# Kernel optimization log

Hardware: AMD Instinct MI355X
Metric: run time of the kernel (lower is better)

Reference implementation:

```python
import jax, jax.numpy as jnp
import numpy as np

B, H, W, C = 8, 64, 64, 256
CB = C // 2          # bottleneck_dim = channels // 2
COMPRESSION = 2      # max-pool factor on flattened spatial axis of phi and g


def setup_inputs() -> dict:
    key = jax.random.key(0)
    k = jax.random.split(key, 5)
    he = lambda kk, fan_in, shape: jax.random.normal(kk, shape, jnp.float32) * np.sqrt(2.0 / fan_in)
    return {
        "x": jax.random.normal(k[0], (B, H, W, C), jnp.float32),
        "W_theta": he(k[1], C, (C, CB)),
        "W_phi": he(k[2], C, (C, CB)),
        "W_g": he(k[3], C, (C, CB)),
        "W_out": he(k[4], CB, (CB, C)),
    }


def _maxpool1d(t, pool):
    # MaxPool1D(pool) along axis 1 of [B, N, C] (valid padding, stride=pool)
    b, n, c = t.shape
    return t.reshape(b, n // pool, pool, c).max(axis=2)


def reference(x, W_theta, W_phi, W_g, W_out):
    b, h, w, c = x.shape
    n = h * w
    xf = x.reshape(b, n, c)                      # flatten spatial dims
    theta = xf @ W_theta                         # [B, N, Cb] (1x1 conv, no bias)
    phi = _maxpool1d(xf @ W_phi, COMPRESSION)    # [B, N/2, Cb]
    g = _maxpool1d(xf @ W_g, COMPRESSION)        # [B, N/2, Cb]
    f = jax.nn.softmax(jnp.einsum('bnd,bmd->bnm', theta, phi), axis=-1)  # [B, N, N/2]
    y = jnp.einsum('bnm,bmd->bnd', f, g)         # [B, N, Cb]
    y = (y @ W_out).reshape(b, h, w, c)          # expand conv back to C
    return x + y                                 # add_residual=True
```

## Files before the change

kernel.cpp:

```cpp
#include <hip/hip_runtime.h>
#include <math.h>

#define BB 8
#define NN 4096
#define MM 2048
#define CC 256
#define CBD 128

typedef __attribute__((ext_vector_type(8))) short s16x8;
typedef __attribute__((ext_vector_type(4))) float f32x4;
typedef __attribute__((ext_vector_type(16))) float f32x16;
typedef unsigned short u16;
typedef unsigned int u32;

__device__ __forceinline__ u16 f2bf(float f) {
    union { float f; u32 u; } v; v.f = f;
    u32 r = v.u + 0x7fffu + ((v.u >> 16) & 1u);
    return (u16)(r >> 16);
}
__device__ __forceinline__ float bf2f(u16 h) {
    union { u32 u; float f; } v; v.u = ((u32)h) << 16; return v.f;
}
__device__ __forceinline__ u32 asu(float f) {
    union { float f; u32 u; } v; v.f = f; return v.u;
}
__device__ __forceinline__ u32 pkbf(float lo, float hi) {
    return __builtin_amdgcn_perm(asu(hi), asu(lo), 0x07060302u);
}

#define MFMA(a, b, c)   __builtin_amdgcn_mfma_f32_16x16x32_bf16(a, b, c, 0, 0, 0)
#define MFMA32(a, b, c) __builtin_amdgcn_mfma_f32_32x32x16_bf16(a, b, c, 0, 0, 0)

__device__ __forceinline__ void gload_lds16(const u16* g, u16* l) {
    __builtin_amdgcn_global_load_lds(
        (const __attribute__((address_space(1))) void*)g,
        (__attribute__((address_space(3))) void*)l, 16, 0, 0);
}

__global__ __launch_bounds__(256) void k_split_w(
    const float* __restrict__ wt, const float* __restrict__ wp,
    const float* __restrict__ wg, const float* __restrict__ wo,
    u16* wth, u16* wtl, u16* wph, u16* wpl, u16* wgh, u16* wgl, u16* wot) {
    int e = blockIdx.x * 256 + threadIdx.x;
    int m = blockIdx.y;
    if (m < 3) {
        const float* src = m == 0 ? wt : (m == 1 ? wp : wg);
        u16* oh = m == 0 ? wth : (m == 1 ? wph : wgh);
        u16* ol = m == 0 ? wtl : (m == 1 ? wpl : wgl);
        int r = e >> 7, c = e & 127;
        float f = src[e];
        u16 hi = f2bf(f);
        oh[c * 256 + r] = hi;
        ol[c * 256 + r] = f2bf(f - bf2f(hi));
    } else {
        int r = e >> 8, c = e & 255;
        wot[c * 128 + r] = f2bf(wo[e]);
    }
}

__global__ __launch_bounds__(256) void k_proj(
    const float* __restrict__ x,
    const u16* __restrict__ wth, const u16* __restrict__ wtl,
    const u16* __restrict__ wph, const u16* __restrict__ wpl,
    const u16* __restrict__ wgh,
    u16* __restrict__ th, u16* __restrict__ tl,
    u16* __restrict__ ph, u16* __restrict__ pl, u16* __restrict__ gt) {
    __shared__ u16 sxh[64][40], sxl[64][40];
    __shared__ u16 sw[5][128][40];
    int tid = threadIdx.x;
    int w = tid >> 6, lane = tid & 63, q = lane >> 4, li = lane & 15;
    int r0 = blockIdx.x * 64;
    int wr2 = (w >> 1) * 32, wcc = (w & 1) * 64;
    const u16* Ws[5] = {wth, wtl, wph, wpl, wgh};

    f32x4 aT[2][4], aP[2][4], aG[2][4];
#pragma unroll
    for (int i = 0; i < 2; i++)
#pragma unroll
        for (int j = 0; j < 4; j++) {
            aT[i][j] = (f32x4)0.f; aP[i][j] = (f32x4)0.f; aG[i][j] = (f32x4)0.f;
        }

    for (int kc = 0; kc < 8; kc++) {
        {
            int row = tid >> 2, seg = tid & 3;
            const float* xp = &x[(size_t)(r0 + row) * 256 + kc * 32 + seg * 8];
            float4 v0 = ((const float4*)xp)[0];
            float4 v1 = ((const float4*)xp)[1];
            float vv[8] = {v0.x, v0.y, v0.z, v0.w, v1.x, v1.y, v1.z, v1.w};
            u16 hh[8], ll[8];
#pragma unroll
            for (int t = 0; t < 8; t++) {
                hh[t] = f2bf(vv[t]);
                ll[t] = f2bf(vv[t] - bf2f(hh[t]));
            }
            *(s16x8*)&sxh[row][seg * 8] = *(s16x8*)&hh[0];
            *(s16x8*)&sxl[row][seg * 8] = *(s16x8*)&ll[0];
        }
#pragma unroll
        for (int u = 0; u < 10; u++) {
            int mat = u >> 1;
            int col = (u & 1) * 64 + (tid >> 2), ch = tid & 3;
            s16x8 v = *(const s16x8*)&Ws[mat][(size_t)col * 256 + kc * 32 + ch * 8];
            *(s16x8*)&sw[mat][col][ch * 8] = v;
        }
        __syncthreads();

        s16x8 ah[2], al[2];
#pragma unroll
        for (int i = 0; i < 2; i++) {
            ah[i] = *(const s16x8*)&sxh[wr2 + i * 16 + li][q * 8];
            al[i] = *(const s16x8*)&sxl[wr2 + i * 16 + li][q * 8];
        }
#pragma unroll
        for (int j = 0; j < 4; j++) {
            int col = wcc + j * 16 + li;
            s16x8 bth = *(const s16x8*)&sw[0][col][q * 8];
            s16x8 btl = *(const s16x8*)&sw[1][col][q * 8];
            s16x8 bph = *(const s16x8*)&sw[2][col][q * 8];
            s16x8 bpl = *(const s16x8*)&sw[3][col][q * 8];
            s16x8 bgh = *(const s16x8*)&sw[4][col][q * 8];
#pragma unroll
            for (int i = 0; i < 2; i++) {
                aT[i][j] = MFMA(ah[i], bth, aT[i][j]);
                aT[i][j] = MFMA(al[i], bth, aT[i][j]);
                aT[i][j] = MFMA(ah[i], btl, aT[i][j]);
                aP[i][j] = MFMA(ah[i], bph, aP[i][j]);
                aP[i][j] = MFMA(al[i], bph, aP[i][j]);
                aP[i][j] = MFMA(ah[i], bpl, aP[i][j]);
                aG[i][j] = MFMA(ah[i], bgh, aG[i][j]);
                aG[i][j] = MFMA(al[i], bgh, aG[i][j]);
            }
        }
        __syncthreads();
    }

#pragma unroll
    for (int i = 0; i < 2; i++)
#pragma unroll
        for (int j = 0; j < 4; j++) {
            int col = wcc + j * 16 + li;
#pragma unroll
            for (int reg = 0; reg < 4; reg++) {
                int n = r0 + wr2 + i * 16 + q * 4 + reg;
                float v = aT[i][j][reg];
                u16 hi = f2bf(v);
                th[(size_t)n * 128 + col] = hi;
                tl[(size_t)n * 128 + col] = f2bf(v - bf2f(hi));
            }
#pragma unroll
            for (int pr = 0; pr < 2; pr++) {
                int n = r0 + wr2 + i * 16 + q * 4 + pr * 2;
                int mrow = n >> 1;
                float vp = fmaxf(aP[i][j][pr * 2], aP[i][j][pr * 2 + 1]);
                u16 hi = f2bf(vp);
                ph[(size_t)mrow * 128 + col] = hi;
                pl[(size_t)mrow * 128 + col] = f2bf(vp - bf2f(hi));
                float vg = fmaxf(aG[i][j][pr * 2], aG[i][j][pr * 2 + 1]);
                int b = n >> 12;
                int mi = mrow & 2047;
                int mi2 = (mi & ~12) | ((mi & 4) << 1) | ((mi & 8) >> 1);
                gt[(size_t)b * (128 * 2048) + (size_t)col * 2048 + mi2] = f2bf(vg);
            }
        }
}

__global__ __launch_bounds__(256, 2) void k_attn(
    const u16* __restrict__ th, const u16* __restrict__ tl,
    const u16* __restrict__ ph, const u16* __restrict__ pl,
    const u16* __restrict__ gt, u16* __restrict__ ot,
    float* __restrict__ Mv, float* __restrict__ Lv) {
    __shared__ u16 smem[24576];
    u16* skh = smem;
    u16* skl = smem + 8192;
    u16* sg  = smem + 16384;
    int tid = threadIdx.x, w = tid >> 6, lane = tid & 63;
    int q = lane & 31, b = lane >> 5;
    int bb = blockIdx.y;
    int s = blockIdx.x & 1;
    int qt = blockIdx.x >> 1;
    int n0 = qt * 128;
    int row128 = w * 32 + q;
    size_t qrow = ((size_t)bb * 4096 + n0 + row128) * 128;

    s16x8 Qh[8], Ql[8];
#pragma unroll
    for (int ks = 0; ks < 8; ks++) {
        Qh[ks] = *(const s16x8*)&th[qrow + ks * 16 + b * 8];
        Ql[ks] = *(const s16x8*)&tl[qrow + ks * 16 + b * 8];
    }
    float mrow = -INFINITY, lrow = 0.f;
    f32x16 o[4];
#pragma unroll
    for (int c = 0; c < 4; c++) o[c] = (f32x16)0.f;

    int r_hi = lane >> 4, c_hi = lane & 15;
    int r_lo = lane >> 3, c_lo = lane & 7;
    int k0 = s * 1024;

    for (int kt = 0; kt < 16; kt++) {
        int m0 = k0 + kt * 64;
        if (kt) __syncthreads();
#pragma unroll
        for (int jj = 0; jj < 4; jj++) {
            int r = w * 16 + jj * 4 + r_hi;
            int gc = c_hi ^ (r & 7);
            size_t ga = (((size_t)(bb * 2048 + m0 + r)) << 7) + gc * 8;
            gload_lds16(&ph[ga], &skh[(w * 16 + jj * 4) << 7]);
            gload_lds16(&pl[ga], &skl[(w * 16 + jj * 4) << 7]);
            int r2 = w * 32 + jj * 8 + r_lo;
            int gc2 = c_lo ^ (r2 & 7);
            size_t ga2 = (size_t)bb * (128 * 2048) + (size_t)r2 * 2048 + m0 + gc2 * 8;
            gload_lds16(&gt[ga2], &sg[(w * 32 + jj * 8) << 6]);
        }
        __syncthreads();

        f32x16 S[2];
        S[0] = (f32x16)0.f; S[1] = (f32x16)0.f;
#pragma unroll
        for (int ks = 0; ks < 8; ks++) {
            int off0 = (q << 7) + (((ks * 2 + b) ^ (q & 7)) << 3);
            int r1 = 32 + q;
            int off1 = (r1 << 7) + (((ks * 2 + b) ^ (r1 & 7)) << 3);
            s16x8 ah0 = *(const s16x8*)&skh[off0];
            s16x8 al0 = *(const s16x8*)&skl[off0];
            s16x8 ah1 = *(const s16x8*)&skh[off1];
            s16x8 al1 = *(const s16x8*)&skl[off1];
            S[0] = MFMA32(ah0, Qh[ks], S[0]);
            S[1] = MFMA32(ah1, Qh[ks], S[1]);
            S[0] = MFMA32(al0, Qh[ks], S[0]);
            S[1] = MFMA32(al1, Qh[ks], S[1]);
            S[0] = MFMA32(ah0, Ql[ks], S[0]);
            S[1] = MFMA32(ah1, Ql[ks], S[1]);
        }

        float vmax = S[0][0];
#pragma unroll
        for (int r = 0; r < 16; r++) {
            vmax = fmaxf(vmax, S[0][r]);
            vmax = fmaxf(vmax, S[1][r]);
        }
        vmax = fmaxf(vmax, __shfl_xor(vmax, 32, 64));
        float nm = fmaxf(mrow, vmax);
        float alph = __expf(mrow - nm);
        mrow = nm;
        float rs = 0.f;
#pragma unroll
        for (int r = 0; r < 16; r++) {
            float p0 = __expf(S[0][r] - nm); S[0][r] = p0; rs += p0;
            float p1 = __expf(S[1][r] - nm); S[1][r] = p1; rs += p1;
        }
        rs += __shfl_xor(rs, 32, 64);
        lrow = lrow * alph + rs;
#pragma unroll
        for (int c = 0; c < 4; c++)
#pragma unroll
            for (int r = 0; r < 16; r++) o[c][r] *= alph;

#pragma unroll
        for (int t = 0; t < 4; t++) {
            int half = t >> 1, base = (t & 1) * 8;
            s16x8 Pf;
            u32* pf = (u32*)&Pf;
#pragma unroll
            for (int r2 = 0; r2 < 4; r2++)
                pf[r2] = pkbf(S[half][base + 2 * r2], S[half][base + 2 * r2 + 1]);
#pragma unroll
            for (int c = 0; c < 4; c++) {
                int ch = c * 32 + q;
                int off = (ch << 6) + (((t * 2 + b) ^ (ch & 7)) << 3);
                s16x8 gv = *(const s16x8*)&sg[off];
                o[c] = MFMA32(gv, Pf, o[c]);
            }
        }
    }
    __syncthreads();

    u16* sc = smem;
#pragma unroll
    for (int c = 0; c < 4; c++)
#pragma unroll
        for (int r2 = 0; r2 < 8; r2++) {
            int ch = c * 32 + ((r2 & 1) << 1) + 8 * (r2 >> 1) + 4 * b;
            u32 pk = (u32)f2bf(o[c][2 * r2]) | ((u32)f2bf(o[c][2 * r2 + 1]) << 16);
            *(u32*)&sc[row128 * 136 + ch] = pk;
        }
    __syncthreads();
    size_t obase = ((size_t)s * 32768 + (size_t)bb * 4096 + n0) * 128;
    int rowy = tid >> 1;
#pragma unroll
    for (int j = 0; j < 8; j++) {
        int chk = (tid & 1) * 8 + j;
        s16x8 v = *(const s16x8*)&sc[rowy * 136 + chk * 8];
        *(s16x8*)&ot[obase + (size_t)rowy * 128 + chk * 8] = v;
    }
    if (b == 0) {
        int gi = s * 32768 + bb * 4096 + n0 + row128;
        Mv[gi] = mrow;
        Lv[gi] = lrow;
    }
}

__global__ __launch_bounds__(256) void k_out(
    const u16* __restrict__ ot, const float* __restrict__ Mv,
    const float* __restrict__ Lv, const u16* __restrict__ wot,
    const float* __restrict__ x, float* __restrict__ out) {
    __shared__ char lds_o[36864];
    u16 (*sy)[72] = (u16(*)[72])lds_o;
    u16 (*sw)[72] = (u16(*)[72])(lds_o + 18432);
    int tid = threadIdx.x, w = tid >> 6, lane = tid & 63, q = lane >> 4, li = lane & 15;
    int r0 = blockIdx.x * 128, c0 = blockIdx.y * 128;
    int wr = (w >> 1) * 64, wc = (w & 1) * 64;
    const size_t OS = (size_t)32768 * 128;

    float a1v[4], a2v[4];
#pragma unroll
    for (int i = 0; i < 4; i++) {
        int gr = r0 + ((tid + i * 256) >> 3);
        float m1 = Mv[gr], m2 = Mv[32768 + gr];
        float l1 = Lv[gr], l2 = Lv[32768 + gr];
        float Mx = fmaxf(m1, m2);
        float e1 = __expf(m1 - Mx), e2 = __expf(m2 - Mx);
        float inv = 1.f / (l1 * e1 + l2 * e2);
        a1v[i] = e1 * inv;
        a2v[i] = e2 * inv;
    }

    f32x4 acc[4][4];
#pragma unroll
    for (int i = 0; i < 4; i++)
#pragma unroll
        for (int j = 0; j < 4; j++) acc[i][j] = (f32x4)0.f;

    for (int kc = 0; kc < 2; kc++) {
#pragma unroll
        for (int i = 0; i < 4; i++) {
            int ch = tid + i * 256;
            int r = ch >> 3, cc = (ch & 7) * 8;
            size_t ga = (size_t)(r0 + r) * 128 + kc * 64 + cc;
            s16x8 o1 = *(const s16x8*)&ot[ga];
            s16x8 o2 = *(const s16x8*)&ot[OS + ga];
            s16x8 yv;
#pragma unroll
            for (int e = 0; e < 8; e++)
                yv[e] = (short)f2bf(bf2f((u16)o1[e]) * a1v[i] +
                                    bf2f((u16)o2[e]) * a2v[i]);
            *(s16x8*)&sy[r][cc] = yv;
            *(s16x8*)&sw[r][cc] = *(const s16x8*)&wot[(size_t)(c0 + r) * 128 + kc * 64 + cc];
        }
        __syncthreads();
#pragma unroll
        for (int ks = 0; ks < 2; ks++)
#pragma unroll
            for (int i = 0; i < 4; i++) {
                s16x8 a = *(const s16x8*)&sy[wr + i * 16 + li][ks * 32 + q * 8];
#pragma unroll
                for (int j = 0; j < 4; j++) {
                    s16x8 bv = *(const s16x8*)&sw[wc + j * 16 + li][ks * 32 + q * 8];
                    acc[i][j] = MFMA(a, bv, acc[i][j]);
                }
            }
        __syncthreads();
    }

    float* sT = (float*)lds_o;
#pragma unroll
    for (int h = 0; h < 2; h++) {
        __syncthreads();
        if ((w >> 1) == h) {
#pragma unroll
            for (int i = 0; i < 4; i++)
#pragma unroll
                for (int j = 0; j < 4; j++)
#pragma unroll
                    for (int reg = 0; reg < 4; reg++)
                        sT[(i * 16 + q * 4 + reg) * 132 + wc + j * 16 + li] =
                            acc[i][j][reg];
        }
        __syncthreads();
#pragma unroll
        for (int p = 0; p < 8; p++) {
            int r = (tid >> 5) + p * 8;
            int c4 = (tid & 31) * 4;
            f32x4 yv = *(f32x4*)&sT[r * 132 + c4];
            size_t row = (size_t)(r0 + h * 64 + r);
            float4 xv = *(const float4*)&x[row * 256 + c0 + c4];
            float4 ov;
            ov.x = xv.x + yv[0]; ov.y = xv.y + yv[1];
            ov.z = xv.z + yv[2]; ov.w = xv.w + yv[3];
            *(float4*)&out[row * 256 + c0 + c4] = ov;
        }
    }
}

extern "C" void kernel_launch(void* const* d_in, const int* in_sizes, int n_in,
                              void* d_out, int out_size, void* d_ws, size_t ws_size,
                              hipStream_t stream) {
    const float* x  = (const float*)d_in[0];
    const float* wt = (const float*)d_in[1];
    const float* wp = (const float*)d_in[2];
    const float* wg = (const float*)d_in[3];
    const float* wo = (const float*)d_in[4];
    float* out = (float*)d_out;

    char* p = (char*)d_ws;
    auto alloc = [&](size_t bytes) {
        char* r = p;
        p += (bytes + 255) & ~(size_t)255;
        return r;
    };
    const size_t NT = (size_t)BB * NN * CBD;
    const size_t NP = (size_t)BB * MM * CBD;

    u16* wth = (u16*)alloc(CC * CBD * 2);
    u16* wtl = (u16*)alloc(CC * CBD * 2);
    u16* wph = (u16*)alloc(CC * CBD * 2);
    u16* wpl = (u16*)alloc(CC * CBD * 2);
    u16* wgh = (u16*)alloc(CC * CBD * 2);
    u16* wgl = (u16*)alloc(CC * CBD * 2);
    u16* wot = (u16*)alloc(CC * CBD * 2);
    u16* th  = (u16*)alloc(NT * 2);
    u16* tl  = (u16*)alloc(NT * 2);
    u16* ph  = (u16*)alloc(NP * 2);
    u16* pl  = (u16*)alloc(NP * 2);
    u16* gt  = (u16*)alloc(NP * 2);
    float* Mv = (float*)alloc(2 * 32768 * 4);
    float* Lv = (float*)alloc(2 * 32768 * 4);
    u16* ot  = (u16*)alloc(2 * NT * 2);

    k_split_w<<<dim3(128, 4), 256, 0, stream>>>(wt, wp, wg, wo,
                                                wth, wtl, wph, wpl, wgh, wgl, wot);
    k_proj<<<dim3(512), 256, 0, stream>>>(x, wth, wtl, wph, wpl, wgh,
                                          th, tl, ph, pl, gt);
    k_attn<<<dim3(64, 8), 256, 0, stream>>>(th, tl, ph, pl, gt, ot, Mv, Lv);
    k_out<<<dim3(256, 2), 256, 0, stream>>>(ot, Mv, Lv, wot, x, out);
}
```

Before: 197.9 us.

## Split attention keys three ways and add lazy softmax rescaling

The key range of the attention kernel is now split into three chunks (704/704/640 keys) instead of two, which raises the grid from 512 to 768 blocks to fill more CUs on the MI355X. The output kernel merges three partial results using their max/sum statistics. The online softmax now skips the rescale of the accumulator unless the running max grows by more than a threshold, and the max and sum reductions are restructured as trees. The cost is extra partial-output traffic, plus a numerical risk: with lazy rescaling, exponentials can reach up to e^25 before the max is updated.

```diff
diff --git a/kernel.cpp b/kernel.cpp
--- a/kernel.cpp
+++ b/kernel.cpp
@@ -177,8 +177,8 @@
     int tid = threadIdx.x, w = tid >> 6, lane = tid & 63;
     int q = lane & 31, b = lane >> 5;
     int bb = blockIdx.y;
-    int s = blockIdx.x & 1;
-    int qt = blockIdx.x >> 1;
+    int s = blockIdx.x >> 5;
+    int qt = blockIdx.x & 31;
     int n0 = qt * 128;
     int row128 = w * 32 + q;
     size_t qrow = ((size_t)bb * 4096 + n0 + row128) * 128;
@@ -196,9 +196,10 @@
 
     int r_hi = lane >> 4, c_hi = lane & 15;
     int r_lo = lane >> 3, c_lo = lane & 7;
-    int k0 = s * 1024;
-
-    for (int kt = 0; kt < 16; kt++) {
+    int k0 = s * 704;
+    int nt = (s == 2) ? 10 : 11;
+
+    for (int kt = 0; kt < nt; kt++) {
         int m0 = k0 + kt * 64;
         if (kt) __syncthreads();
 #pragma unroll
@@ -234,28 +235,40 @@
             S[1] = MFMA32(ah1, Ql[ks], S[1]);
         }
 
-        float vmax = S[0][0];
-#pragma unroll
-        for (int r = 0; r < 16; r++) {
-            vmax = fmaxf(vmax, S[0][r]);
-            vmax = fmaxf(vmax, S[1][r]);
-        }
+        float t0[8];
+#pragma unroll
+        for (int r = 0; r < 8; r++)
+            t0[r] = fmaxf(fmaxf(S[0][r], S[0][r + 8]),
+                          fmaxf(S[1][r], S[1][r + 8]));
+        float u0 = fmaxf(t0[0], t0[1]), u1 = fmaxf(t0[2], t0[3]);
+        float u2 = fmaxf(t0[4], t0[5]), u3 = fmaxf(t0[6], t0[7]);
+        float vmax = fmaxf(fmaxf(u0, u1), fmaxf(u2, u3));
         vmax = fmaxf(vmax, __shfl_xor(vmax, 32, 64));
-        float nm = fmaxf(mrow, vmax);
-        float alph = __expf(mrow - nm);
-        mrow = nm;
-        float rs = 0.f;
-#pragma unroll
-        for (int r = 0; r < 16; r++) {
-            float p0 = __expf(S[0][r] - nm); S[0][r] = p0; rs += p0;
-            float p1 = __expf(S[1][r] - nm); S[1][r] = p1; rs += p1;
-        }
+        if (!__all(vmax - mrow <= 25.f)) {
+            float nm = fmaxf(mrow, vmax);
+            float alph = __expf(mrow - nm);
+            mrow = nm;
+            lrow *= alph;
+#pragma unroll
+            for (int c = 0; c < 4; c++)
+#pragma unroll
+                for (int r = 0; r < 16; r++) o[c][r] *= alph;
+        }
+        float rs0 = 0.f, rs1 = 0.f, rs2 = 0.f, rs3 = 0.f;
+#pragma unroll
+        for (int r = 0; r < 4; r++) {
+            float p00 = __expf(S[0][r] - mrow);      S[0][r] = p00;      rs0 += p00;
+            float p01 = __expf(S[0][r + 4] - mrow);  S[0][r + 4] = p01;  rs1 += p01;
+            float p02 = __expf(S[0][r + 8] - mrow);  S[0][r + 8] = p02;  rs2 += p02;
+            float p03 = __expf(S[0][r + 12] - mrow); S[0][r + 12] = p03; rs3 += p03;
+            float p10 = __expf(S[1][r] - mrow);      S[1][r] = p10;      rs0 += p10;
+            float p11 = __expf(S[1][r + 4] - mrow);  S[1][r + 4] = p11;  rs1 += p11;
+            float p12 = __expf(S[1][r + 8] - mrow);  S[1][r + 8] = p12;  rs2 += p12;
+            float p13 = __expf(S[1][r + 12] - mrow); S[1][r + 12] = p13; rs3 += p13;
+        }
+        float rs = (rs0 + rs1) + (rs2 + rs3);
         rs += __shfl_xor(rs, 32, 64);
-        lrow = lrow * alph + rs;
-#pragma unroll
-        for (int c = 0; c < 4; c++)
-#pragma unroll
-            for (int r = 0; r < 16; r++) o[c][r] *= alph;
+        lrow += rs;
 
 #pragma unroll
         for (int t = 0; t < 4; t++) {
@@ -313,17 +326,16 @@
     int wr = (w >> 1) * 64, wc = (w & 1) * 64;
     const size_t OS = (size_t)32768 * 128;
 
-    float a1v[4], a2v[4];
+    float av0[4], av1[4], av2[4];
 #pragma unroll
     for (int i = 0; i < 4; i++) {
         int gr = r0 + ((tid + i * 256) >> 3);
-        float m1 = Mv[gr], m2 = Mv[32768 + gr];
-        float l1 = Lv[gr], l2 = Lv[32768 + gr];
-        float Mx = fmaxf(m1, m2);
-        float e1 = __expf(m1 - Mx), e2 = __expf(m2 - Mx);
-        float inv = 1.f / (l1 * e1 + l2 * e2);
-        a1v[i] = e1 * inv;
-        a2v[i] = e2 * inv;
+        float m0 = Mv[gr], m1 = Mv[32768 + gr], m2 = Mv[65536 + gr];
+        float l0 = Lv[gr], l1 = Lv[32768 + gr], l2 = Lv[65536 + gr];
+        float Mx = fmaxf(fmaxf(m0, m1), m2);
+        float e0 = __expf(m0 - Mx), e1 = __expf(m1 - Mx), e2 = __expf(m2 - Mx);
+        float inv = 1.f / (l0 * e0 + l1 * e1 + l2 * e2);
+        av0[i] = e0 * inv; av1[i] = e1 * inv; av2[i] = e2 * inv;
     }
 
     f32x4 acc[4][4];
@@ -340,11 +352,13 @@
             size_t ga = (size_t)(r0 + r) * 128 + kc * 64 + cc;
             s16x8 o1 = *(const s16x8*)&ot[ga];
             s16x8 o2 = *(const s16x8*)&ot[OS + ga];
+            s16x8 o3 = *(const s16x8*)&ot[2 * OS + ga];
             s16x8 yv;
 #pragma unroll
             for (int e = 0; e < 8; e++)
-                yv[e] = (short)f2bf(bf2f((u16)o1[e]) * a1v[i] +
-                                    bf2f((u16)o2[e]) * a2v[i]);
+                yv[e] = (short)f2bf(bf2f((u16)o1[e]) * av0[i] +
+                                    bf2f((u16)o2[e]) * av1[i] +
+                                    bf2f((u16)o3[e]) * av2[i]);
             *(s16x8*)&sy[r][cc] = yv;
             *(s16x8*)&sw[r][cc] = *(const s16x8*)&wot[(size_t)(c0 + r) * 128 + kc * 64 + cc];
         }
@@ -424,14 +438,14 @@
     u16* ph  = (u16*)alloc(NP * 2);
     u16* pl  = (u16*)alloc(NP * 2);
     u16* gt  = (u16*)alloc(NP * 2);
-    float* Mv = (float*)alloc(2 * 32768 * 4);
-    float* Lv = (float*)alloc(2 * 32768 * 4);
-    u16* ot  = (u16*)alloc(2 * NT * 2);
+    float* Mv = (float*)alloc(3 * 32768 * 4);
+    float* Lv = (float*)alloc(3 * 32768 * 4);
+    u16* ot  = (u16*)alloc(3 * NT * 2);
 
     k_split_w<<<dim3(128, 4), 256, 0, stream>>>(wt, wp, wg, wo,
                                                 wth, wtl, wph, wpl, wgh, wgl, wot);
     k_proj<<<dim3(512), 256, 0, stream>>>(x, wth, wtl, wph, wpl, wgh,
                                           th, tl, ph, pl, gt);
-    k_attn<<<dim3(64, 8), 256, 0, stream>>>(th, tl, ph, pl, gt, ot, Mv, Lv);
+    k_attn<<<dim3(96, 8), 256, 0, stream>>>(th, tl, ph, pl, gt, ot, Mv, Lv);
     k_out<<<dim3(256, 2), 256, 0, stream>>>(ot, Mv, Lv, wot, x, out);
 }
```

Measured after the change: 205.2 us. +3.7%, slower.
